# Performance work log

Hardware: AMD Instinct MI355X
Metric: run time of the kernel (lower is better)

The kernel has to match this reference:

```python
import jax, jax.numpy as jnp
import numpy as np

SHIFT, REDUCE = 1, 2
B, L, E, H = 128, 64, 512, 512
T = 2 * L - 1  # valid binary-parse transition sequence length


def _make_transitions(rng):
    # Random *valid* shift-reduce sequences: L shifts, L-1 reduces, stack ends at 1.
    trans = np.zeros((B, T), dtype=np.int32)
    for b in range(B):
        stack, buf = 0, L
        for t in range(T):
            ops_left = T - t
            can_shift = buf > 0 and stack < ops_left
            can_reduce = stack >= 2
            if can_shift and can_reduce:
                act = SHIFT if rng.random() < 0.5 else REDUCE
            elif can_shift:
                act = SHIFT
            else:
                act = REDUCE
            if act == SHIFT:
                buf -= 1; stack += 1
            else:
                stack -= 1
            trans[b, t] = act
    return trans


def setup_inputs() -> dict:
    key = jax.random.key(0)
    k1, k2, k3, k4 = jax.random.split(key, 4)
    sentence = jax.random.normal(k1, (B, L, E), dtype=jnp.float32)
    transitions = jnp.asarray(_make_transitions(np.random.default_rng(0)))
    W_word = jax.random.normal(k2, (E, 2 * H), dtype=jnp.float32) / np.sqrt(E).astype(np.float32)
    b_word = jnp.zeros((2 * H,), dtype=jnp.float32)
    W_left = jax.random.normal(k3, (H, 5 * H), dtype=jnp.float32) / np.sqrt(H).astype(np.float32)
    W_right = jax.random.normal(k4, (H, 5 * H), dtype=jnp.float32) / np.sqrt(H).astype(np.float32)
    b_reduce = jnp.zeros((5 * H,), dtype=jnp.float32)
    return {"sentence": sentence, "transitions": transitions, "W_word": W_word,
            "b_word": b_word, "W_left": W_left, "W_right": W_right, "b_reduce": b_reduce}


def reference(sentence, transitions, W_word, b_word, W_left, W_right, b_reduce):
    Bx, Lx, _ = sentence.shape
    Hx = W_left.shape[0]
    Tx = transitions.shape[1]
    # word projection (no_batch_norm=True, dropout=0 in this config)
    out = sentence @ W_word + b_word                      # [B, L, 2H]
    h_buf, c_buf = jnp.split(out, 2, axis=2)              # buffers, popped front-to-back
    rows = jnp.arange(Bx)
    ops_left_seq = jnp.arange(Tx, 0, -1, dtype=jnp.int32)
    init = (jnp.zeros((Bx, Lx, Hx), out.dtype),           # stack h
            jnp.zeros((Bx, Lx, Hx), out.dtype),           # stack c
            jnp.zeros((Bx,), jnp.int32),                  # stack ptr
            jnp.zeros((Bx,), jnp.int32))                  # buffer ptr

    def step(carry, xs):
        sh, sc, sp, bp = carry
        act, ops = xs
        act = jnp.where(sp > ops, REDUCE, act)            # forced reduce (discrete stack)
        is_red = act == REDUCE
        is_shf = act == SHIFT
        r_idx = jnp.clip(sp - 1, 0, Lx - 1)
        l_idx = jnp.clip(sp - 2, 0, Lx - 1)
        hl, cl = sh[rows, l_idx], sc[rows, l_idx]
        hr, cr = sh[rows, r_idx], sc[rows, r_idx]
        # TreeLSTM Reduce cell
        gates = hl @ W_left + hr @ W_right + b_reduce     # [B, 5H]
        g, i, f1, f2, o = jnp.split(gates, 5, axis=1)
        c_red = jnp.tanh(g) * jax.nn.sigmoid(i) + jax.nn.sigmoid(f1) * cl + jax.nn.sigmoid(f2) * cr
        h_red = jax.nn.sigmoid(o) * jnp.tanh(c_red)
        b_idx = jnp.clip(bp, 0, Lx - 1)
        h_shf, c_shf = h_buf[rows, b_idx], c_buf[rows, b_idx]
        w_idx = jnp.where(is_red, l_idx, jnp.clip(sp, 0, Lx - 1))
        h_cur, c_cur = sh[rows, w_idx], sc[rows, w_idx]
        m_red, m_shf = is_red[:, None], is_shf[:, None]
        wh = jnp.where(m_red, h_red, jnp.where(m_shf, h_shf, h_cur))
        wc = jnp.where(m_red, c_red, jnp.where(m_shf, c_shf, c_cur))
        sh = sh.at[rows, w_idx].set(wh)
        sc = sc.at[rows, w_idx].set(wc)
        sp = sp + is_shf.astype(jnp.int32) - is_red.astype(jnp.int32)
        bp = bp + is_shf.astype(jnp.int32)
        return (sh, sc, sp, bp), None

    (sh, sc, sp, bp), _ = jax.lax.scan(step, init, (transitions.T, ops_left_seq))
    return sh[rows, jnp.clip(sp - 1, 0, Lx - 1)]          # [B, H] top of each stack
```

## Files before the change

kernel.cpp:

```cpp
#include <hip/hip_runtime.h>
#include <hip/hip_bf16.h>


#define Bn 128
#define Ln 64
#define En 512
#define Hn 512
#define Tn 127
#define LEAF_ROWS (Bn*Ln)
#define NODE_ROWS (Bn*(Ln-1))
#define TOT_ROWS (LEAF_ROWS+NODE_ROWS)
#define NLVL 64
#define NXCD 8
#define CAPX 512
#define NBLK 512
#define FPAD 16
#define MAXRANK 96
#define SPIN_CAP (1<<22)
#define WLDS_BYTES 65536
#define PART_BYTES (4*2*16*20*4)
#define DYN_BYTES (WLDS_BYTES + PART_BYTES)

#define OFF_CENSUS 0
#define OFF_RANK   (OFF_CENSUS + NXCD*FPAD)
#define OFF_SFLAG  (OFF_RANK + NBLK*FPAD)
#define OFF_SGEN   (OFF_SFLAG + NBLK*FPAD)
#define OFF_FX     (OFF_SGEN + FPAD)
#define OFF_GX     (OFF_FX + NXCD*MAXRANK*FPAD)
#define BAR_INTS   (OFF_GX + NXCD*FPAD)

typedef __attribute__((ext_vector_type(8))) short bf16x8;
typedef __attribute__((ext_vector_type(4))) float f32x4;

static __device__ __forceinline__ float bf2f(unsigned short u){
  unsigned v = ((unsigned)u) << 16;
  float f; __builtin_memcpy(&f, &v, 4); return f;
}
static __device__ __forceinline__ unsigned short f2bf(float f){
  unsigned u; __builtin_memcpy(&u, &f, 4);
  u = u + 0x7FFFu + ((u >> 16) & 1u);
  return (unsigned short)(u >> 16);
}
static __device__ __forceinline__ float sigm(float x){
  return 1.0f / (1.0f + __expf(-x));
}
static __device__ __forceinline__ float tanh_fast(float x){
  x = fminf(fmaxf(x, -15.0f), 15.0f);
  float t = __expf(2.0f * x);
  return (t - 1.0f) / (t + 1.0f);
}
static __device__ __forceinline__ int xcc_id(){
  unsigned v;
  asm volatile("s_getreg_b32 %0, hwreg(HW_REG_XCC_ID)" : "=s"(v));
  return (int)(v & 7);
}

static __device__ __forceinline__ void xcd_barrier(int* bar, int x, int rank, int nx, int epoch){
  __syncthreads();
  int* fx = bar + OFF_FX + x * MAXRANK * FPAD;
  int* gx = bar + OFF_GX + x * FPAD;
  int nxl = min(nx, MAXRANK);
  if (rank == 0){
    for (int i = threadIdx.x + 1; i < nxl; i += 256){
      int c = 0;
      while (__hip_atomic_load(&fx[i * FPAD], __ATOMIC_RELAXED, __HIP_MEMORY_SCOPE_AGENT) < epoch && c < SPIN_CAP){
        __builtin_amdgcn_s_sleep(1); ++c;
      }
    }
    __syncthreads();
    if (threadIdx.x == 0)
      __hip_atomic_store(gx, epoch, __ATOMIC_RELAXED, __HIP_MEMORY_SCOPE_AGENT);
  } else {
    if (threadIdx.x == 0){
      __hip_atomic_store(&fx[rank * FPAD], epoch, __ATOMIC_RELAXED, __HIP_MEMORY_SCOPE_AGENT);
      int c = 0;
      while (__hip_atomic_load(gx, __ATOMIC_RELAXED, __HIP_MEMORY_SCOPE_AGENT) < epoch && c < SPIN_CAP){
        __builtin_amdgcn_s_sleep(2); ++c;
      }
    }
    __syncthreads();
  }
  asm volatile("" ::: "memory");
}


__global__ void cvt_vec4(const float4* __restrict__ x, ushort4* __restrict__ y, int n4){
  int i = blockIdx.x * 256 + threadIdx.x;
  if (i < n4){
    float4 v = x[i];
    ushort4 o;
    o.x = f2bf(v.x); o.y = f2bf(v.y); o.z = f2bf(v.z); o.w = f2bf(v.w);
    y[i] = o;
  }
}

__global__ void transpose_cvt(const float* __restrict__ src, unsigned short* __restrict__ dstT,
                              int CS, int DS, int koff){
  __shared__ float tile[32][33];
  int c0 = blockIdx.x * 32, r0 = blockIdx.y * 32;
  int tx = threadIdx.x, ty = threadIdx.y;
  for (int i = ty; i < 32; i += 8) tile[i][tx] = src[(size_t)(r0 + i) * CS + c0 + tx];
  __syncthreads();
  for (int i = ty; i < 32; i += 8)
    dstT[(size_t)(c0 + i) * DS + koff + r0 + tx] = f2bf(tile[tx][i]);
}

__global__ void precompute_ctrl(const int* __restrict__ trans,
                                int* __restrict__ srcL, int* __restrict__ srcR,
                                int* __restrict__ dstv, int* __restrict__ cnt,
                                int* __restrict__ outsrc, int* __restrict__ bar){
  __shared__ int stk[Bn][Ln + 1];
  __shared__ int scnt[NXCD * NLVL];
  __shared__ int smaxl[NXCD];
  int b = threadIdx.x;
  for (int i = b; i < NXCD * NLVL; i += 128) scnt[i] = 0;
  if (b < NXCD) smaxl[b] = 0;
  for (int i = b; i < BAR_INTS; i += 128) bar[i] = 0;
  __syncthreads();
  int x = b & 7;
  int sp = 0, bp = 0, nodecnt = 0;
  int act_next = trans[b * Tn];
  for (int t = 0; t < Tn; t++){
    int act = act_next;
    if (t + 1 < Tn) act_next = trans[b * Tn + t + 1];
    int ops = Tn - t;
    if (sp > ops) act = 2;
    if (act == 2){
      int R = stk[b][sp - 1], L = stk[b][sp - 2];
      int lvl = max(R >> 20, L >> 20) + 1;
      int slot = atomicAdd(&scnt[x * NLVL + lvl], 1);
      int base = (x * NLVL + lvl) * CAPX + slot;
      srcL[base] = (L & 0xFFFFF) * Hn;
      srcR[base] = (R & 0xFFFFF) * Hn;
      int noderow = LEAF_ROWS + b * (Ln - 1) + nodecnt;
      dstv[base] = noderow * Hn;
      stk[b][sp - 2] = noderow | (lvl << 20);
      sp -= 1; nodecnt++;
    } else {
      stk[b][sp] = b * Ln + min(bp, Ln - 1);
      sp += 1; bp += 1;
    }
  }
  int root = stk[b][max(sp - 1, 0)];
  outsrc[b] = (root & 0xFFFFF) * Hn;
  atomicMax(&smaxl[x], root >> 20);
  __syncthreads();
  for (int i = b; i < NXCD * NLVL; i += 128) cnt[i] = scnt[i];
  if (b < NXCD) cnt[NXCD * NLVL + b] = smaxl[b];
}

__global__ __launch_bounds__(256) void word_gemm(
    const unsigned short* __restrict__ SB, const unsigned short* __restrict__ WwT,
    const float* __restrict__ b_word,
    unsigned short* __restrict__ HB, float* __restrict__ CF){
  int nt = blockIdx.x;
  int mt = blockIdx.y;
  int tid = threadIdx.x, w = tid >> 6, lane = tid & 63;
  int wm = w >> 1, wn = w & 1;
  int rc = lane & 15, lg = lane >> 4;
  const unsigned short* ap0 = SB + (size_t)(mt * 64 + wm * 32 + rc) * En + lg * 8;
  const unsigned short* ap1 = ap0 + (size_t)16 * En;
  const unsigned short* bp0 = WwT + (size_t)(nt * 128 + wn * 64 + rc) * En + lg * 8;
  f32x4 acc[2][4];
  #pragma unroll
  for (int h = 0; h < 2; h++)
    #pragma unroll
    for (int nb = 0; nb < 4; nb++) acc[h][nb] = (f32x4){0.f,0.f,0.f,0.f};
  #pragma unroll 4
  for (int k0 = 0; k0 < En; k0 += 32){
    bf16x8 a0 = *(const bf16x8*)(ap0 + k0);
    bf16x8 a1 = *(const bf16x8*)(ap1 + k0);
    #pragma unroll
    for (int nb = 0; nb < 4; nb++){
      bf16x8 bb = *(const bf16x8*)(bp0 + (size_t)nb * 16 * En + k0);
      acc[0][nb] = __builtin_amdgcn_mfma_f32_16x16x32_bf16(a0, bb, acc[0][nb], 0, 0, 0);
      acc[1][nb] = __builtin_amdgcn_mfma_f32_16x16x32_bf16(a1, bb, acc[1][nb], 0, 0, 0);
    }
  }
  #pragma unroll
  for (int nb = 0; nb < 4; nb++){
    int col = nt * 128 + wn * 64 + nb * 16 + rc;
    float bw = b_word[col];
    #pragma unroll
    for (int h = 0; h < 2; h++){
      #pragma unroll
      for (int q = 0; q < 4; q++){
        int row = mt * 64 + wm * 32 + h * 16 + lg * 4 + q;
        float v = acc[h][nb][q] + bw;
        if (col < Hn) HB[(size_t)row * Hn + col] = f2bf(v);
        else          CF[(size_t)row * Hn + (col - Hn)] = v;
      }
    }
  }
}

template<bool LDSB>
static __device__ __forceinline__ void tile64(
    int u0, int t, int nr, const int* __restrict__ sL, const int* __restrict__ sR,
    const int* __restrict__ dl,
    unsigned short* __restrict__ HB, float* __restrict__ CF,
    const unsigned short* __restrict__ WT, const float* __restrict__ b_red,
    const unsigned short* __restrict__ wlds, int rc, int lg)
{
  int base = t * 64;
  int offL[4], offR[4];
  #pragma unroll
  for (int m = 0; m < 4; m++){
    int i = min(base + m * 16 + rc, nr - 1);
    offL[m] = sL[i]; offR[m] = sR[i];
  }
  f32x4 acc[5][4];
  #pragma unroll
  for (int g = 0; g < 5; g++)
    #pragma unroll
    for (int m = 0; m < 4; m++) acc[g][m] = (f32x4){0.f,0.f,0.f,0.f};

  int bswz = (rc & 7) << 3;
  const unsigned short* gb = WT + (size_t)(u0 + rc) * 1024 + lg * 8;

  bf16x8 a_cur[4], b_cur[3];
  #pragma unroll
  for (int m = 0; m < 4; m++) a_cur[m] = *(const bf16x8*)(HB + offL[m] + lg * 8);
  #pragma unroll
  for (int g = 0; g < 3; g++)
    b_cur[g] = *(const bf16x8*)(gb + (size_t)(g + 2) * (512 * 1024));

  #pragma unroll 4
  for (int j = 0; j < 32; ++j){
    bf16x8 a_nxt[4], b_nxt[3];
    if (j < 31){
      int kn = (j + 1) * 32 + lg * 8;
      #pragma unroll
      for (int m = 0; m < 4; m++){
        const unsigned short* ap = (j + 1 < 16) ? (HB + offL[m] + kn) : (HB + offR[m] + (kn - 512));
        a_nxt[m] = *(const bf16x8*)ap;
      }
      #pragma unroll
      for (int g = 0; g < 3; g++)
        b_nxt[g] = *(const bf16x8*)(gb + (size_t)(g + 2) * (512 * 1024) + (j + 1) * 32);
    }
    int k = j * 32 + lg * 8;
    #pragma unroll
    for (int g = 0; g < 2; g++){
      bf16x8 bb;
      if (LDSB) bb = *(const bf16x8*)&wlds[(size_t)(g * 16 + rc) * 1024 + (k ^ bswz)];
      else      bb = *(const bf16x8*)(gb + (size_t)g * (512 * 1024) + j * 32);
      #pragma unroll
      for (int m = 0; m < 4; m++)
        acc[g][m] = __builtin_amdgcn_mfma_f32_16x16x32_bf16(a_cur[m], bb, acc[g][m], 0, 0, 0);
    }
    #pragma unroll
    for (int g = 0; g < 3; g++){
      #pragma unroll
      for (int m = 0; m < 4; m++)
        acc[g + 2][m] = __builtin_amdgcn_mfma_f32_16x16x32_bf16(a_cur[m], b_cur[g], acc[g + 2][m], 0, 0, 0);
    }
    #pragma unroll
    for (int m = 0; m < 4; m++) a_cur[m] = a_nxt[m];
    #pragma unroll
    for (int g = 0; g < 3; g++) b_cur[g] = b_nxt[g];
  }
  int colu = u0 + rc;
  float bs[5];
  #pragma unroll
  for (int g = 0; g < 5; g++) bs[g] = b_red[g * Hn + colu];
  #pragma unroll
  for (int m = 0; m < 4; m++){
    #pragma unroll
    for (int q = 0; q < 4; q++){
      int i = base + m * 16 + lg * 4 + q;
      if (i < nr){
        int oL = sL[i], oR = sR[i], oD = dl[i];
        float gv = tanh_fast(acc[0][m][q] + bs[0]);
        float iv = sigm(acc[1][m][q] + bs[1]);
        float f1 = sigm(acc[2][m][q] + bs[2]);
        float f2 = sigm(acc[3][m][q] + bs[3]);
        float ov = sigm(acc[4][m][q] + bs[4]);
        float cl = __builtin_nontemporal_load(CF + oL + colu);
        float cr = __builtin_nontemporal_load(CF + oR + colu);
        float cv = gv * iv + f1 * cl + f2 * cr;
        float hv = ov * tanh_fast(cv);
        __builtin_nontemporal_store(cv, CF + oD + colu);
        HB[oD + colu] = f2bf(hv);
      }
    }
  }
}

static __device__ __forceinline__ void tile16(
    int u0, int t, int nr, const int* __restrict__ sL, const int* __restrict__ sR,
    const int* __restrict__ dl,
    unsigned short* __restrict__ HB, float* __restrict__ CF,
    const unsigned short* __restrict__ WT, const float* __restrict__ b_red,
    const unsigned short* __restrict__ wlds, float (*part)[2][16][20],
    int tid, int w, int rc, int lg)
{
  int base = t * 16;
  int i0 = min(base + rc, nr - 1);
  int offA = (w >= 2) ? sR[i0] : sL[i0];
  int k0 = w * 256;
  int abase = (w >= 2) ? (k0 - 512) : k0;
  const unsigned short* ap = HB + offA + abase + lg * 8;
  int bswz = (rc & 7) << 3;
  const unsigned short* gb = WT + (size_t)(u0 + rc) * 1024;

  f32x4 acc[5];
  #pragma unroll
  for (int g = 0; g < 5; g++) acc[g] = (f32x4){0.f,0.f,0.f,0.f};

  bf16x8 a_cur = *(const bf16x8*)ap;
  bf16x8 b_cur[3];
  #pragma unroll
  for (int g = 0; g < 3; g++)
    b_cur[g] = *(const bf16x8*)(gb + (size_t)(g + 2) * (512 * 1024) + k0 + lg * 8);

  #pragma unroll
  for (int j = 0; j < 8; ++j){
    bf16x8 a_nxt, b_nxt[3];
    if (j < 7){
      a_nxt = *(const bf16x8*)(ap + (j + 1) * 32);
      #pragma unroll
      for (int g = 0; g < 3; g++)
        b_nxt[g] = *(const bf16x8*)(gb + (size_t)(g + 2) * (512 * 1024) + k0 + (j + 1) * 32 + lg * 8);
    }
    int k = k0 + j * 32 + lg * 8;
    #pragma unroll
    for (int g = 0; g < 2; g++){
      bf16x8 bb = *(const bf16x8*)&wlds[(size_t)(g * 16 + rc) * 1024 + (k ^ bswz)];
      acc[g] = __builtin_amdgcn_mfma_f32_16x16x32_bf16(a_cur, bb, acc[g], 0, 0, 0);
    }
    #pragma unroll
    for (int g = 0; g < 3; g++)
      acc[g + 2] = __builtin_amdgcn_mfma_f32_16x16x32_bf16(a_cur, b_cur[g], acc[g + 2], 0, 0, 0);
    a_cur = a_nxt;
    #pragma unroll
    for (int g = 0; g < 3; g++) b_cur[g] = b_nxt[g];
  }
  int er = tid >> 4, eu = tid & 15;
  float sg[5];
  #pragma unroll
  for (int r = 0; r < 3; ++r){
    int ng = (r < 2) ? 2 : 1;
    #pragma unroll
    for (int gi = 0; gi < 2; ++gi){
      if (gi < ng){
        int g = r * 2 + gi;
        #pragma unroll
        for (int q = 0; q < 4; q++) part[w][gi][lg * 4 + q][rc] = acc[g][q];
      }
    }
    __syncthreads();
    #pragma unroll
    for (int gi = 0; gi < 2; ++gi){
      if (gi < ng)
        sg[r * 2 + gi] = part[0][gi][er][eu] + part[1][gi][er][eu]
                       + part[2][gi][er][eu] + part[3][gi][er][eu];
    }
    __syncthreads();
  }
  int i = base + er;
  if (i < nr){
    int colu = u0 + eu;
    int oL = sL[i], oR = sR[i], oD = dl[i];
    float gv = tanh_fast(sg[0] + b_red[colu]);
    float iv = sigm(sg[1] + b_red[Hn + colu]);
    float f1 = sigm(sg[2] + b_red[2 * Hn + colu]);
    float f2 = sigm(sg[3] + b_red[3 * Hn + colu]);
    float ov = sigm(sg[4] + b_red[4 * Hn + colu]);
    float cl = __builtin_nontemporal_load(CF + oL + colu);
    float cr = __builtin_nontemporal_load(CF + oR + colu);
    float cv = gv * iv + f1 * cl + f2 * cr;
    float hv = ov * tanh_fast(cv);
    __builtin_nontemporal_store(cv, CF + oD + colu);
    HB[oD + colu] = f2bf(hv);
  }
  __syncthreads();
}

extern __shared__ char dynbuf[];

__global__ __launch_bounds__(256, 2) void tree_kernel(
    unsigned short* __restrict__ HB, float* __restrict__ CF,
    const unsigned short* __restrict__ WT, const float* __restrict__ b_red,
    const int* __restrict__ srcL, const int* __restrict__ srcR,
    const int* __restrict__ dstv, const int* __restrict__ cnt,
    const int* __restrict__ outsrc, float* __restrict__ out, int* bar){
  unsigned short* wlds = (unsigned short*)dynbuf;
  float (*part)[2][16][20] = (float(*)[2][16][20])(dynbuf + WLDS_BYTES);
  int bid = blockIdx.x;
  int tid = threadIdx.x, w = tid >> 6, lane = tid & 63;
  int rc = lane & 15, lg = lane >> 4;

  int x = xcc_id();
  if (tid == 0){
    int r = __hip_atomic_fetch_add(&bar[OFF_CENSUS + x * FPAD], 1,
                                   __ATOMIC_RELAXED, __HIP_MEMORY_SCOPE_AGENT);
    __hip_atomic_store(&bar[OFF_RANK + bid * FPAD], r, __ATOMIC_RELAXED, __HIP_MEMORY_SCOPE_AGENT);
  }
  __syncthreads();
  int rank = min(__hip_atomic_load(&bar[OFF_RANK + bid * FPAD], __ATOMIC_RELAXED, __HIP_MEMORY_SCOPE_AGENT),
                 MAXRANK - 1);
  int ub = rank & 31;
  int u0 = ub * 16;

  for (int gg = tid; gg < 4096; gg += 256){
    int row = gg >> 7;
    int k = (gg & 127) * 8;
    int u = row & 15, g = row >> 4;
    bf16x8 v = *(const bf16x8*)(WT + (size_t)(g * 512 + u0 + u) * 1024 + k);
    int kx = k ^ ((u & 7) << 3);
    *(bf16x8*)&wlds[(size_t)row * 1024 + kx] = v;
  }
  __syncthreads();

  {
    int* sfl  = bar + OFF_SFLAG;
    int* sgen = bar + OFF_SGEN;
    if (bid == 0){
      for (int i = tid; i < NBLK; i += 256){
        if (i){
          int c = 0;
          while (__hip_atomic_load(&sfl[i * FPAD], __ATOMIC_RELAXED, __HIP_MEMORY_SCOPE_AGENT) == 0 && c < SPIN_CAP){
            __builtin_amdgcn_s_sleep(1); ++c;
          }
        }
      }
      __syncthreads();
      if (tid == 0) __hip_atomic_store(sgen, 1, __ATOMIC_RELAXED, __HIP_MEMORY_SCOPE_AGENT);
    } else {
      if (tid == 0){
        __hip_atomic_store(&sfl[bid * FPAD], 1, __ATOMIC_RELAXED, __HIP_MEMORY_SCOPE_AGENT);
        int c = 0;
        while (__hip_atomic_load(sgen, __ATOMIC_RELAXED, __HIP_MEMORY_SCOPE_AGENT) == 0 && c < SPIN_CAP){
          __builtin_amdgcn_s_sleep(2); ++c;
        }
      }
      __syncthreads();
    }
  }
  int nx = max(__hip_atomic_load(&bar[OFF_CENSUS + x * FPAD], __ATOMIC_RELAXED, __HIP_MEMORY_SCOPE_AGENT), 1);

  int maxlvl = cnt[NXCD * NLVL + x];
  int epoch = 1;
  for (int lvl = 1; lvl <= maxlvl; ++lvl, ++epoch){
    int nr = cnt[x * NLVL + lvl];
    const int* sL = srcL + (x * NLVL + lvl) * CAPX;
    const int* sR = srcR + (x * NLVL + lvl) * CAPX;
    const int* dl = dstv + (x * NLVL + lvl) * CAPX;
    if (nr > 0){
      if (nx >= 32){
        int nstr = (nx - 1 - ub) / 32 + 1;
        int stripe = rank >> 5;
        if (nr >= 128){
          int ntl = (nr + 63) >> 6;
          for (int t = stripe * 4 + w; t < ntl; t += nstr * 4)
            tile64<true>(u0, t, nr, sL, sR, dl, HB, CF, WT, b_red, wlds, rc, lg);
        } else {
          int ntl16 = (nr + 15) >> 4;
          for (int t = stripe; t < ntl16; t += nstr)
            tile16(u0, t, nr, sL, sR, dl, HB, CF, WT, b_red, wlds, part, tid, w, rc, lg);
        }
      } else {
        int ntl = (nr + 63) >> 6;
        int nwv = nx * 4, wid = rank * 4 + w;
        int ntask = ntl * 32;
        for (int task = wid; task < ntask; task += nwv)
          tile64<false>((task / ntl) * 16, task % ntl, nr, sL, sR, dl, HB, CF, WT, b_red, wlds, rc, lg);
      }
    }
    xcd_barrier(bar, x, rank, nx, epoch);
  }

  for (int j = rank; j < 16; j += min(nx, MAXRANK)){
    int b = x + 8 * j;
    int src = outsrc[b];
    out[b * Hn + tid]       = bf2f(HB[src + tid]);
    out[b * Hn + tid + 256] = bf2f(HB[src + tid + 256]);
  }
}

extern "C" void kernel_launch(void* const* d_in, const int* in_sizes, int n_in,
                              void* d_out, int out_size, void* d_ws, size_t ws_size,
                              hipStream_t stream){
  (void)in_sizes; (void)n_in; (void)out_size; (void)ws_size;
  const float* sentence = (const float*)d_in[0];
  const int*   trans    = (const int*)d_in[1];
  const float* W_word   = (const float*)d_in[2];
  const float* b_word   = (const float*)d_in[3];
  const float* W_left   = (const float*)d_in[4];
  const float* W_right  = (const float*)d_in[5];
  const float* b_red    = (const float*)d_in[6];

  char* ws = (char*)d_ws;
  size_t off = 0;
  auto alloc = [&](size_t bytes) -> void* {
    void* p = ws + off;
    off += (bytes + 255) & ~((size_t)255);
    return p;
  };
  unsigned short* HB  = (unsigned short*)alloc((size_t)TOT_ROWS * Hn * 2);
  float*          CF  = (float*)alloc((size_t)TOT_ROWS * Hn * 4);
  unsigned short* WT  = (unsigned short*)alloc((size_t)2560 * 1024 * 2);
  unsigned short* SB  = (unsigned short*)alloc((size_t)LEAF_ROWS * En * 2);
  unsigned short* WwT = (unsigned short*)alloc((size_t)1024 * En * 2);
  int* srcL   = (int*)alloc((size_t)NXCD * NLVL * CAPX * 4);
  int* srcR   = (int*)alloc((size_t)NXCD * NLVL * CAPX * 4);
  int* dstv   = (int*)alloc((size_t)NXCD * NLVL * CAPX * 4);
  int* cnt    = (int*)alloc((size_t)(NXCD * NLVL + NXCD) * 4);
  int* outsrc = (int*)alloc((size_t)Bn * 4);
  int* bar    = (int*)alloc((size_t)BAR_INTS * 4);
  float* outp = (float*)d_out;

  hipFuncSetAttribute(reinterpret_cast<const void*>(tree_kernel),
                      hipFuncAttributeMaxDynamicSharedMemorySize, DYN_BYTES);

  cvt_vec4<<<(LEAF_ROWS * En / 4) / 256, 256, 0, stream>>>((const float4*)sentence, (ushort4*)SB, LEAF_ROWS * En / 4);
  transpose_cvt<<<dim3(1024 / 32, En / 32), dim3(32, 8), 0, stream>>>(W_word, WwT, 1024, En, 0);
  transpose_cvt<<<dim3(2560 / 32, Hn / 32), dim3(32, 8), 0, stream>>>(W_left, WT, 2560, 1024, 0);
  transpose_cvt<<<dim3(2560 / 32, Hn / 32), dim3(32, 8), 0, stream>>>(W_right, WT, 2560, 1024, 512);
  precompute_ctrl<<<1, 128, 0, stream>>>(trans, srcL, srcR, dstv, cnt, outsrc, bar);
  word_gemm<<<dim3(8, LEAF_ROWS / 64), 256, 0, stream>>>(SB, WwT, b_word, HB, CF);
  tree_kernel<<<NBLK, 256, DYN_BYTES, stream>>>(HB, CF, WT, b_red, srcL, srcR, dstv, cnt, outsrc, outp, bar);
}
```

Measured before the change: 598.3 us.

## Prefetch word GEMM operands, swap grid order, hoist tile16 cell-state loads

```diff
diff --git a/kernel.cpp b/kernel.cpp
--- a/kernel.cpp
+++ b/kernel.cpp
@@ -17,6 +17,7 @@
 #define FPAD 16
 #define MAXRANK 96
 #define SPIN_CAP (1<<22)
+#define GATE_STRIDE (512*1024)
 #define WLDS_BYTES 65536
 #define PART_BYTES (4*2*16*20*4)
 #define DYN_BYTES (WLDS_BYTES + PART_BYTES)
@@ -153,8 +154,8 @@
     const unsigned short* __restrict__ SB, const unsigned short* __restrict__ WwT,
     const float* __restrict__ b_word,
     unsigned short* __restrict__ HB, float* __restrict__ CF){
-  int nt = blockIdx.x;
-  int mt = blockIdx.y;
+  int mt = blockIdx.x;
+  int nt = blockIdx.y;
   int tid = threadIdx.x, w = tid >> 6, lane = tid & 63;
   int wm = w >> 1, wn = w & 1;
   int rc = lane & 15, lg = lane >> 4;
@@ -166,16 +167,32 @@
   for (int h = 0; h < 2; h++)
     #pragma unroll
     for (int nb = 0; nb < 4; nb++) acc[h][nb] = (f32x4){0.f,0.f,0.f,0.f};
-  #pragma unroll 4
-  for (int k0 = 0; k0 < En; k0 += 32){
-    bf16x8 a0 = *(const bf16x8*)(ap0 + k0);
-    bf16x8 a1 = *(const bf16x8*)(ap1 + k0);
+
+  bf16x8 a0c = *(const bf16x8*)ap0;
+  bf16x8 a1c = *(const bf16x8*)ap1;
+  bf16x8 bc[4];
+  #pragma unroll
+  for (int nb = 0; nb < 4; nb++) bc[nb] = *(const bf16x8*)(bp0 + (size_t)nb * 16 * En);
+
+  #pragma unroll
+  for (int j = 0; j < 16; ++j){
+    bf16x8 a0n, a1n, bn[4];
+    if (j < 15){
+      int kn = (j + 1) * 32;
+      a0n = *(const bf16x8*)(ap0 + kn);
+      a1n = *(const bf16x8*)(ap1 + kn);
+      #pragma unroll
+      for (int nb = 0; nb < 4; nb++)
+        bn[nb] = *(const bf16x8*)(bp0 + (size_t)nb * 16 * En + kn);
+    }
     #pragma unroll
     for (int nb = 0; nb < 4; nb++){
-      bf16x8 bb = *(const bf16x8*)(bp0 + (size_t)nb * 16 * En + k0);
-      acc[0][nb] = __builtin_amdgcn_mfma_f32_16x16x32_bf16(a0, bb, acc[0][nb], 0, 0, 0);
-      acc[1][nb] = __builtin_amdgcn_mfma_f32_16x16x32_bf16(a1, bb, acc[1][nb], 0, 0, 0);
-    }
+      acc[0][nb] = __builtin_amdgcn_mfma_f32_16x16x32_bf16(a0c, bc[nb], acc[0][nb], 0, 0, 0);
+      acc[1][nb] = __builtin_amdgcn_mfma_f32_16x16x32_bf16(a1c, bc[nb], acc[1][nb], 0, 0, 0);
+    }
+    a0c = a0n; a1c = a1n;
+    #pragma unroll
+    for (int nb = 0; nb < 4; nb++) bc[nb] = bn[nb];
   }
   #pragma unroll
   for (int nb = 0; nb < 4; nb++){
@@ -223,7 +240,7 @@
   for (int m = 0; m < 4; m++) a_cur[m] = *(const bf16x8*)(HB + offL[m] + lg * 8);
   #pragma unroll
   for (int g = 0; g < 3; g++)
-    b_cur[g] = *(const bf16x8*)(gb + (size_t)(g + 2) * (512 * 1024));
+    b_cur[g] = *(const bf16x8*)(gb + (size_t)(g + 2) * GATE_STRIDE);
 
   #pragma unroll 4
   for (int j = 0; j < 32; ++j){
@@ -237,14 +254,14 @@
       }
       #pragma unroll
       for (int g = 0; g < 3; g++)
-        b_nxt[g] = *(const bf16x8*)(gb + (size_t)(g + 2) * (512 * 1024) + (j + 1) * 32);
+        b_nxt[g] = *(const bf16x8*)(gb + (size_t)(g + 2) * GATE_STRIDE + (j + 1) * 32);
     }
     int k = j * 32 + lg * 8;
     #pragma unroll
     for (int g = 0; g < 2; g++){
       bf16x8 bb;
       if (LDSB) bb = *(const bf16x8*)&wlds[(size_t)(g * 16 + rc) * 1024 + (k ^ bswz)];
-      else      bb = *(const bf16x8*)(gb + (size_t)g * (512 * 1024) + j * 32);
+      else      bb = *(const bf16x8*)(gb + (size_t)g * GATE_STRIDE + j * 32);
       #pragma unroll
       for (int m = 0; m < 4; m++)
         acc[g][m] = __builtin_amdgcn_mfma_f32_16x16x32_bf16(a_cur[m], bb, acc[g][m], 0, 0, 0);
@@ -296,8 +313,15 @@
     int tid, int w, int rc, int lg)
 {
   int base = t * 16;
+  int er = tid >> 4, eu = tid & 15;
   int i0 = min(base + rc, nr - 1);
   int offA = (w >= 2) ? sR[i0] : sL[i0];
+  int ie = min(base + er, nr - 1);
+  int oL = sL[ie], oR = sR[ie], oD = dl[ie];
+  int colu = u0 + eu;
+  float cl = __builtin_nontemporal_load(CF + oL + colu);
+  float cr = __builtin_nontemporal_load(CF + oR + colu);
+
   int k0 = w * 256;
   int abase = (w >= 2) ? (k0 - 512) : k0;
   const unsigned short* ap = HB + offA + abase + lg * 8;
@@ -312,7 +336,7 @@
   bf16x8 b_cur[3];
   #pragma unroll
   for (int g = 0; g < 3; g++)
-    b_cur[g] = *(const bf16x8*)(gb + (size_t)(g + 2) * (512 * 1024) + k0 + lg * 8);
+    b_cur[g] = *(const bf16x8*)(gb + (size_t)(g + 2) * GATE_STRIDE + k0 + lg * 8);
 
   #pragma unroll
   for (int j = 0; j < 8; ++j){
@@ -321,7 +345,7 @@
       a_nxt = *(const bf16x8*)(ap + (j + 1) * 32);
       #pragma unroll
       for (int g = 0; g < 3; g++)
-        b_nxt[g] = *(const bf16x8*)(gb + (size_t)(g + 2) * (512 * 1024) + k0 + (j + 1) * 32 + lg * 8);
+        b_nxt[g] = *(const bf16x8*)(gb + (size_t)(g + 2) * GATE_STRIDE + k0 + (j + 1) * 32 + lg * 8);
     }
     int k = k0 + j * 32 + lg * 8;
     #pragma unroll
@@ -336,7 +360,6 @@
     #pragma unroll
     for (int g = 0; g < 3; g++) b_cur[g] = b_nxt[g];
   }
-  int er = tid >> 4, eu = tid & 15;
   float sg[5];
   #pragma unroll
   for (int r = 0; r < 3; ++r){
@@ -360,15 +383,11 @@
   }
   int i = base + er;
   if (i < nr){
-    int colu = u0 + eu;
-    int oL = sL[i], oR = sR[i], oD = dl[i];
     float gv = tanh_fast(sg[0] + b_red[colu]);
     float iv = sigm(sg[1] + b_red[Hn + colu]);
     float f1 = sigm(sg[2] + b_red[2 * Hn + colu]);
     float f2 = sigm(sg[3] + b_red[3 * Hn + colu]);
     float ov = sigm(sg[4] + b_red[4 * Hn + colu]);
-    float cl = __builtin_nontemporal_load(CF + oL + colu);
-    float cr = __builtin_nontemporal_load(CF + oR + colu);
     float cv = gv * iv + f1 * cl + f2 * cr;
     float hv = ov * tanh_fast(cv);
     __builtin_nontemporal_store(cv, CF + oD + colu);
@@ -519,6 +538,6 @@
   transpose_cvt<<<dim3(2560 / 32, Hn / 32), dim3(32, 8), 0, stream>>>(W_left, WT, 2560, 1024, 0);
   transpose_cvt<<<dim3(2560 / 32, Hn / 32), dim3(32, 8), 0, stream>>>(W_right, WT, 2560, 1024, 512);
   precompute_ctrl<<<1, 128, 0, stream>>>(trans, srcL, srcR, dstv, cnt, outsrc, bar);
-  word_gemm<<<dim3(8, LEAF_ROWS / 64), 256, 0, stream>>>(SB, WwT, b_word, HB, CF);
+  word_gemm<<<dim3(128, 8), 256, 0, stream>>>(SB, WwT, b_word, HB, CF);
   tree_kernel<<<NBLK, 256, DYN_BYTES, stream>>>(HB, CF, WT, b_red, srcL, srcR, dstv, cnt, outsrc, outp, bar);
 }
```

New measurement: 609.0 us. About the same (+1.8%).
